# Performance work log

Hardware: AMD Instinct MI355X
Metric: run time of the kernel (lower is better)

## Reference

```python
import jax, jax.numpy as jnp
import numpy as np

N = 131072
IN_A = 256
IN_V = 512
IN_VF = 512
CH = 256
BN_EPS = 1e-5
COS_EPS = 1e-8


def setup_inputs() -> dict:
    key = jax.random.key(0)
    ks = jax.random.split(key, 12)
    s = 0.05
    return {
        "x": jax.random.normal(ks[0], (N, 4, 512), dtype=jnp.float32),
        "audio_node_mask": jax.random.bernoulli(ks[1], 0.5, (N,)),
        "W_a": jax.random.normal(ks[2], (IN_A, CH), dtype=jnp.float32) * s,
        "b_a": jnp.zeros((CH,), jnp.float32),
        "W_v": jax.random.normal(ks[3], (IN_V, CH), dtype=jnp.float32) * s,
        "b_v": jnp.zeros((CH,), jnp.float32),
        "W_f": jax.random.normal(ks[4], (2 * CH, CH), dtype=jnp.float32) * s,
        "b_f": jnp.zeros((CH,), jnp.float32),
        "gamma": jnp.ones((CH,), jnp.float32),
        "beta": jnp.zeros((CH,), jnp.float32),
        "W_fc": jax.random.normal(ks[5], (CH, 2), dtype=jnp.float32) * s,
        "b_fc": jnp.zeros((2,), jnp.float32),
    }


def reference(x, audio_node_mask, W_a, b_a, W_v, b_v, W_f, b_f, gamma, beta, W_fc, b_fc):
    # Slice per-type features (x: [N, 4, 512])
    a_in = x[:, 0, :IN_A]    # audio feats (also video->audio feats)
    v_in = x[:, 1, :IN_V]    # video feats
    a_vf = x[:, 2, :IN_VF]   # audio voice-face emb
    v_vf = x[:, 3, :IN_VF]   # video voice-face emb

    # cosine similarity along feature dim (torch.nn.functional.cosine_similarity semantics)
    dot = jnp.sum(a_vf * v_vf, axis=1)
    denom = jnp.maximum(jnp.linalg.norm(a_vf, axis=1) * jnp.linalg.norm(v_vf, axis=1), COS_EPS)
    sim = dot / denom  # [N]

    # per-type linears (compute densely, select by mask -> same math as masked scatter)
    a_out = a_in @ W_a + b_a                                   # [N, CH]
    v_out = v_in @ W_v + b_v                                   # [N, CH]
    va = a_in * sim[:, None]                                   # sim-weighted audio feats on video nodes
    fused = jnp.concatenate([va, v_out], axis=1) @ W_f + b_f   # [N, CH]

    graph_feats = jnp.where(audio_node_mask[:, None], a_out, fused)

    # BatchNorm1d (training: batch statistics, biased variance)
    mu = jnp.mean(graph_feats, axis=0)
    var = jnp.mean(jnp.square(graph_feats - mu), axis=0)
    graph_feats = (graph_feats - mu) * jax.lax.rsqrt(var + BN_EPS) * gamma + beta

    graph_feats = jax.nn.relu(graph_feats)
    return graph_feats @ W_fc + b_fc  # [N, 2]
```

## Files before the change

### kernel.cpp

```cpp
#include <hip/hip_runtime.h>
#include <hip/hip_bf16.h>
#include <stdint.h>

#define NN 131072

typedef unsigned int uint;
typedef unsigned short ushort;
typedef __attribute__((ext_vector_type(8))) __bf16 bf16x8;
typedef __attribute__((ext_vector_type(2))) __bf16 bf16x2;
typedef __attribute__((ext_vector_type(4))) float f32x4;


__device__ __forceinline__ ushort f2bf(float f) {
    uint u = __float_as_uint(f);
    u += 0x7FFF + ((u >> 16) & 1);
    return (ushort)(u >> 16);
}
__device__ __forceinline__ uint pk2(float a, float b) {
    bf16x2 t;
    t[0] = (__bf16)a;
    t[1] = (__bf16)b;
    return __builtin_bit_cast(uint, t);
}
__device__ __forceinline__ bool mask_val(const unsigned char* m8, int flag, int i) {
    return flag ? (m8[(size_t)i * 4] != 0) : (m8[i] != 0);
}
__device__ __forceinline__ size_t pack_off(int k, int c) {
    return (size_t)(((k >> 5) * 16 + (c >> 4)) * 512
                    + (((k >> 3) & 3) * 16 + (c & 15)) * 8 + (k & 7));
}

__global__ void k_detect(const uint* m32, int n, int* flag) {
    __shared__ int cnt;
    if (threadIdx.x == 0) cnt = 0;
    __syncthreads();
    int local = 0;
    int nw = n >> 2;
    for (int i = threadIdx.x; i < nw; i += 1024)
        if (m32[i] & 0x0000FF00u) local = 1;
    if (local) atomicAdd(&cnt, 1);
    __syncthreads();
    if (threadIdx.x == 0) *flag = (cnt == 0) ? 1 : 0;
}

__global__ void k_count(const unsigned char* m8, const int* flagp, int* cntM) {
    int flag = *flagp;
    int t = threadIdx.x;
    bool m = mask_val(m8, flag, blockIdx.x * 256 + t);
    unsigned long long bal = __ballot(m);
    __shared__ int wsum[4];
    if ((t & 63) == 0) wsum[t >> 6] = __popcll(bal);
    __syncthreads();
    if (t == 0) cntM[blockIdx.x] = wsum[0] + wsum[1] + wsum[2] + wsum[3];
}

__global__ void k_scan(const int* __restrict__ cntM, int* __restrict__ meta,
                       int* __restrict__ baseA, int* __restrict__ baseF) {
    __shared__ int sA[512], sF[512];
    int t = threadIdx.x;
    int a = cntM[t], f = 256 - a;
    sA[t] = a; sF[t] = f;
    __syncthreads();
    for (int off = 1; off < 512; off <<= 1) {
        int va = (t >= off) ? sA[t - off] : 0;
        int vf = (t >= off) ? sF[t - off] : 0;
        __syncthreads();
        sA[t] += va; sF[t] += vf;
        __syncthreads();
    }
    baseA[t] = sA[t] - a;
    baseF[t] = sF[t] - f;
    if (t == 511) { meta[2] = sA[511]; meta[1] = sF[511]; }
}

__global__ void k_fill(const unsigned char* m8, const int* flagp,
                       const int* __restrict__ baseA, const int* __restrict__ baseF,
                       int* __restrict__ audioIdx, int* __restrict__ fusedIdx) {
    int flag = *flagp;
    int blk = blockIdx.x, t = threadIdx.x;
    int row = blk * 256 + t;
    bool m = mask_val(m8, flag, row);
    unsigned long long bal = __ballot(m);
    int lane = t & 63, w = t >> 6;
    unsigned long long lt = (1ull << lane) - 1ull;
    int pA = __popcll(bal & lt);
    __shared__ int wA[4];
    if (lane == 0) wA[w] = __popcll(bal);
    __syncthreads();
    int offA = 0;
    for (int i = 0; i < w; ++i) offA += wA[i];
    int offF = w * 64 - offA;
    int pF = lane - pA;
    if (m) audioIdx[baseA[blk] + offA + pA] = row;
    else   fusedIdx[baseF[blk] + offF + pF] = row;
}

__global__ void k_prep(const float* __restrict__ Wa, const float* __restrict__ Wf,
                       const float* __restrict__ Wv, const float* __restrict__ bv,
                       const float* __restrict__ bf_, ushort* __restrict__ Bwa,
                       ushort* __restrict__ Bwf, float* __restrict__ cf) {
    int c = threadIdx.x;
    int b = blockIdx.x;
    if (b < 256) {
        Bwa[pack_off(b, c)] = f2bf(Wa[b * 256 + c]);
    } else if (b < 512) {
        Bwf[pack_off(512 + (b - 256), c)] = f2bf(Wf[(b - 256) * 256 + c]);
    } else if (b < 1024) {
        int k = b - 512;
        const float* wr = Wv + k * 256;
        float acc = 0.f;
        for (int j = 0; j < 256; ++j) acc += wr[j] * Wf[(256 + j) * 256 + c];
        Bwf[pack_off(k, c)] = f2bf(acc);
    } else {
        float acc = bf_[c];
        for (int j = 0; j < 256; ++j) acc += bv[j] * Wf[(256 + j) * 256 + c];
        cf[c] = acc;
    }
}

__global__ __launch_bounds__(512, 4) void k_main(
    const float* __restrict__ x, const int* __restrict__ meta,
    const int* __restrict__ fusedIdx, const int* __restrict__ audioIdx,
    const ushort* __restrict__ Bwa, const ushort* __restrict__ Bwf,
    const float* __restrict__ ba, const float* __restrict__ cf,
    ushort* __restrict__ gf, float* __restrict__ bn_s, float* __restrict__ bn_q)
{
    __shared__ bf16x8 As8[2][128 * 8];
    __shared__ int ridxS[128];
    __shared__ float simS[128];
    __shared__ unsigned char validS[128];
    __shared__ float redS[256], redQ[256];

    const int tid = threadIdx.x;
    const int cntF = meta[1], cntA = meta[2];
    const int nbF = (cntF + 127) >> 7;
    const int nbA = (cntA + 127) >> 7;
    const int b = blockIdx.x;
    const bool isF = b < nbF;
    const int bb = isF ? b : b - nbF;

    if (!isF && bb >= nbA) {
        if (tid < 256) {
            bn_s[(size_t)b * 256 + tid] = 0.f;
            bn_q[(size_t)b * 256 + tid] = 0.f;
        }
        return;
    }

    const int cnt = isF ? cntF : cntA;
    const int* idxArr = isF ? fusedIdx : audioIdx;
    const int lane = tid & 63;
    const int w = tid >> 6, wr = w >> 2, wc = w & 3;
    const int fr = lane & 15, fg = lane >> 4;

    if (tid < 128) {
        int gpos = bb * 128 + tid;
        int ok = gpos < cnt;
        ridxS[tid] = ok ? idxArr[gpos] : 0;
        validS[tid] = ok;
        simS[tid] = 1.f;
    }
    __syncthreads();

    const int NS = isF ? 12 : 4;
    const int sr = tid >> 2, sk = tid & 3;
    const float* xrow = x + (size_t)ridxS[sr] * 2048;
    const float sVf = validS[sr] ? 1.f : 0.f;
    float sAf = 0.f;

    int4 pA_A[2], pA_B[2];
    auto loadA = [&](int st, int4* p) {
        const float scl = (isF && st >= 8) ? sAf : sVf;
        const int off = isF ? ((st < 8) ? 512 + st * 64 : (st - 8) * 64) : st * 64;
        const float4* src = (const float4*)(xrow + off + sk * 16);
        #pragma unroll
        for (int s = 0; s < 2; ++s) {
            float4 u0 = src[2 * s], u1 = src[2 * s + 1];
            int4 q;
            q.x = pk2(u0.x * scl, u0.y * scl);
            q.y = pk2(u0.z * scl, u0.w * scl);
            q.z = pk2(u1.x * scl, u1.y * scl);
            q.w = pk2(u1.z * scl, u1.w * scl);
            p[s] = q;
        }
    };
    auto storeA = [&](int buf, const int4* p) {
        #pragma unroll
        for (int s = 0; s < 2; ++s)
            As8[buf][sr * 8 + ((sk * 2 + s) ^ (sr & 7))] = __builtin_bit_cast(bf16x8, p[s]);
    };

    const ushort* bBase = (isF ? Bwf : Bwa) + ((size_t)(wc * 4) << 9) + (lane << 3);

    f32x4 acc[4][4];
    #pragma unroll
    for (int m = 0; m < 4; ++m)
        #pragma unroll
        for (int n = 0; n < 4; ++n) acc[m][n] = (f32x4){0.f, 0.f, 0.f, 0.f};

    auto compute = [&](int buf, int st) {
        #pragma unroll
        for (int kk = 0; kk < 2; ++kk) {
            bf16x8 af[4];
            #pragma unroll
            for (int m = 0; m < 4; ++m) {
                int r = wr * 64 + m * 16 + fr;
                af[m] = As8[buf][r * 8 + ((kk * 4 + fg) ^ (r & 7))];
            }
            #pragma unroll
            for (int n = 0; n < 4; ++n) {
                bf16x8 bv = *(const bf16x8*)(bBase + ((size_t)((st * 2 + kk) * 16 + n) << 9));
                #pragma unroll
                for (int m = 0; m < 4; ++m)
                    acc[m][n] = __builtin_amdgcn_mfma_f32_16x16x32_bf16(
                        af[m], bv, acc[m][n], 0, 0, 0);
            }
        }
    };

    loadA(0, pA_A);

    if (isF) {
        #pragma unroll 2
        for (int rr = 0; rr < 16; ++rr) {
            int r = w * 16 + rr;
            const float4* p = (const float4*)(x + (size_t)ridxS[r] * 2048 + 1024);
            float4 a0 = p[lane], a1 = p[lane + 64];
            float4 v0 = p[lane + 128], v1 = p[lane + 192];
            float dot = a0.x * v0.x + a0.y * v0.y + a0.z * v0.z + a0.w * v0.w
                      + a1.x * v1.x + a1.y * v1.y + a1.z * v1.z + a1.w * v1.w;
            float na = a0.x * a0.x + a0.y * a0.y + a0.z * a0.z + a0.w * a0.w
                     + a1.x * a1.x + a1.y * a1.y + a1.z * a1.z + a1.w * a1.w;
            float nv = v0.x * v0.x + v0.y * v0.y + v0.z * v0.z + v0.w * v0.w
                     + v1.x * v1.x + v1.y * v1.y + v1.z * v1.z + v1.w * v1.w;
            #pragma unroll
            for (int off = 32; off; off >>= 1) {
                dot += __shfl_xor(dot, off);
                na  += __shfl_xor(na,  off);
                nv  += __shfl_xor(nv,  off);
            }
            if (lane == 0)
                simS[r] = dot / fmaxf(sqrtf(na) * sqrtf(nv), 1e-8f);
        }
    }
    __syncthreads();
    sAf = validS[sr] ? simS[sr] : 0.f;

    storeA(0, pA_A);
    loadA(1, pA_B);
    __syncthreads();

    for (int st = 0; st < NS; st += 2) {
        if (st + 2 < NS) loadA(st + 2, pA_A);
        compute(0, st);
        storeA(1, pA_B);
        __syncthreads();
        if (st + 3 < NS) loadA(st + 3, pA_B);
        compute(1, st + 1);
        if (st + 2 < NS) storeA(0, pA_A);
        __syncthreads();
    }

    if (tid < 256) { redS[tid] = 0.f; redQ[tid] = 0.f; }
    __syncthreads();

    const int colLo = wc * 64 + fr;
    const float* biasp = isF ? cf : ba;
    float bN[4];
    #pragma unroll
    for (int n = 0; n < 4; ++n) bN[n] = biasp[colLo + n * 16];

    float cs[4] = {0.f, 0.f, 0.f, 0.f}, cq[4] = {0.f, 0.f, 0.f, 0.f};
    #pragma unroll
    for (int m = 0; m < 4; ++m) {
        #pragma unroll
        for (int j = 0; j < 4; ++j) {
            int rloc = wr * 64 + m * 16 + fg * 4 + j;
            if (!validS[rloc]) continue;
            ushort* grow = gf + (size_t)ridxS[rloc] * 256;
            #pragma unroll
            for (int n = 0; n < 4; ++n) {
                float g = acc[m][n][j] + bN[n];
                grow[colLo + n * 16] = f2bf(g);
                cs[n] += g;
                cq[n] += g * g;
            }
        }
    }
    #pragma unroll
    for (int n = 0; n < 4; ++n) {
        atomicAdd(&redS[colLo + n * 16], cs[n]);
        atomicAdd(&redQ[colLo + n * 16], cq[n]);
    }
    __syncthreads();
    if (tid < 256) {
        bn_s[(size_t)b * 256 + tid] = redS[tid];
        bn_q[(size_t)b * 256 + tid] = redQ[tid];
    }
}

__global__ void k_stats(const float* __restrict__ bn_s, const float* __restrict__ bn_q,
                        const float* __restrict__ gamma, const float* __restrict__ beta,
                        float* __restrict__ scale, float* __restrict__ shift) {
    int c = blockIdx.x;
    int t = threadIdx.x;
    float s = 0.f, q = 0.f;
    for (int r = t; r < 1025; r += 256) {
        s += bn_s[(size_t)r * 256 + c];
        q += bn_q[(size_t)r * 256 + c];
    }
    __shared__ float ss[256], qq[256];
    ss[t] = s; qq[t] = q;
    __syncthreads();
    for (int off = 128; off; off >>= 1) {
        if (t < off) { ss[t] += ss[t + off]; qq[t] += qq[t + off]; }
        __syncthreads();
    }
    if (t == 0) {
        float mu  = ss[0] / 131072.f;
        float var = qq[0] / 131072.f - mu * mu;
        float sc = gamma[c] * rsqrtf(var + 1e-5f);
        scale[c] = sc;
        shift[c] = beta[c] - mu * sc;
    }
}

__global__ void k_out(const ushort* __restrict__ gf, const float* __restrict__ scale,
                      const float* __restrict__ shift, const float* __restrict__ Wfc,
                      const float* __restrict__ bfc, float* __restrict__ out) {
    int wid = threadIdx.x >> 6;
    int lane = threadIdx.x & 63;
    int i = blockIdx.x * 4 + wid;
    uint2 gv = ((const uint2*)(gf + (size_t)i * 256))[lane];
    float g0 = __uint_as_float(gv.x << 16);
    float g1 = __uint_as_float(gv.x & 0xFFFF0000u);
    float g2 = __uint_as_float(gv.y << 16);
    float g3 = __uint_as_float(gv.y & 0xFFFF0000u);
    int c0 = lane * 4;
    float4 sc = *(const float4*)(scale + c0);
    float4 sh = *(const float4*)(shift + c0);
    float y0 = fmaxf(g0 * sc.x + sh.x, 0.f);
    float y1 = fmaxf(g1 * sc.y + sh.y, 0.f);
    float y2 = fmaxf(g2 * sc.z + sh.z, 0.f);
    float y3 = fmaxf(g3 * sc.w + sh.w, 0.f);
    const float4* w = (const float4*)(Wfc + c0 * 2);
    float4 w0 = w[0], w1 = w[1];
    float p0 = y0 * w0.x + y1 * w0.z + y2 * w1.x + y3 * w1.z;
    float p1 = y0 * w0.y + y1 * w0.w + y2 * w1.y + y3 * w1.w;
    #pragma unroll
    for (int off = 32; off; off >>= 1) {
        p0 += __shfl_xor(p0, off);
        p1 += __shfl_xor(p1, off);
    }
    if (lane == 0) {
        out[(size_t)i * 2]     = p0 + bfc[0];
        out[(size_t)i * 2 + 1] = p1 + bfc[1];
    }
}

extern "C" void kernel_launch(void* const* d_in, const int* in_sizes, int n_in,
                              void* d_out, int out_size, void* d_ws, size_t ws_size,
                              hipStream_t stream) {
    const float* x          = (const float*)d_in[0];
    const unsigned char* mk = (const unsigned char*)d_in[1];
    const float* Wa  = (const float*)d_in[2];
    const float* ba  = (const float*)d_in[3];
    const float* Wv  = (const float*)d_in[4];
    const float* bv  = (const float*)d_in[5];
    const float* Wf  = (const float*)d_in[6];
    const float* bf  = (const float*)d_in[7];
    const float* gamma = (const float*)d_in[8];
    const float* beta  = (const float*)d_in[9];
    const float* Wfc = (const float*)d_in[10];
    const float* bfc = (const float*)d_in[11];
    float* out = (float*)d_out;

    char* ws = (char*)d_ws;
    int*    meta   = (int*)ws;
    float*  scale  = (float*)(ws + 1024);
    float*  shift  = (float*)(ws + 2048);
    float*  cf     = (float*)(ws + 3072);
    int*    cntM   = (int*)(ws + 8192);
    int*    baseA  = (int*)(ws + 12288);
    int*    baseF  = (int*)(ws + 16384);
    ushort* Bwa    = (ushort*)(ws + 32768);
    ushort* Bwf    = (ushort*)(ws + 262144);
    int*    fusedIdx = (int*)(ws + (1u << 20));
    int*    audioIdx = (int*)(ws + (1u << 20) + (512u << 10));
    float*  bn_s   = (float*)(ws + (2u << 20));
    float*  bn_q   = (float*)(ws + (4u << 20));
    ushort* gf     = (ushort*)(ws + (8u << 20));

    int n = in_sizes[1];

    k_detect<<<1, 1024, 0, stream>>>((const uint*)mk, n, meta);
    k_count<<<512, 256, 0, stream>>>(mk, meta, cntM);
    k_scan<<<1, 512, 0, stream>>>(cntM, meta, baseA, baseF);
    k_fill<<<512, 256, 0, stream>>>(mk, meta, baseA, baseF, audioIdx, fusedIdx);
    k_prep<<<1025, 256, 0, stream>>>(Wa, Wf, Wv, bv, bf, Bwa, Bwf, cf);
    k_main<<<1025, 512, 0, stream>>>(x, meta, fusedIdx, audioIdx, Bwa, Bwf, ba, cf,
                                     gf, bn_s, bn_q);
    k_stats<<<256, 256, 0, stream>>>(bn_s, bn_q, gamma, beta, scale, shift);
    k_out<<<NN / 4, 256, 0, stream>>>(gf, scale, shift, Wfc, bfc, out);
}
```

Measured before the change: 245.1 us.

## Interleave cosine-sim with GEMM pipeline, stage output via LDS, vectorize mask detect

The cosine-similarity computation for fused rows is split into chunks and interleaved with the first seven K-steps of the bf16 MFMA main loop, so the similarity loads overlap with the matrix work instead of running before it. The double-buffer loop is rewritten with one register staging set and a single barrier per step. Output rows are staged through LDS and written to the gf buffer as 32-byte contiguous stores per row, replacing scattered 2-byte stores. The mask-detect kernel reads 16 bytes per thread instead of 4. The LDS staging adds extra barriers in the epilogue.

```diff
diff --git a/kernel.cpp b/kernel.cpp
--- a/kernel.cpp
+++ b/kernel.cpp
@@ -30,14 +30,16 @@
                     + (((k >> 3) & 3) * 16 + (c & 15)) * 8 + (k & 7));
 }
 
-__global__ void k_detect(const uint* m32, int n, int* flag) {
+__global__ void k_detect(const uint4* m128, int n, int* flag) {
     __shared__ int cnt;
     if (threadIdx.x == 0) cnt = 0;
     __syncthreads();
     int local = 0;
-    int nw = n >> 2;
-    for (int i = threadIdx.x; i < nw; i += 1024)
-        if (m32[i] & 0x0000FF00u) local = 1;
+    int nv = n >> 4;
+    for (int i = threadIdx.x; i < nv; i += 1024) {
+        uint4 v = m128[i];
+        if ((v.x | v.y | v.z | v.w) & 0x0000FF00u) local = 1;
+    }
     if (local) atomicAdd(&cnt, 1);
     __syncthreads();
     if (threadIdx.x == 0) *flag = (cnt == 0) ? 1 : 0;
@@ -168,8 +170,8 @@
     const float sVf = validS[sr] ? 1.f : 0.f;
     float sAf = 0.f;
 
-    int4 pA_A[2], pA_B[2];
-    auto loadA = [&](int st, int4* p) {
+    int4 pA[2];
+    auto loadA = [&](int st) {
         const float scl = (isF && st >= 8) ? sAf : sVf;
         const int off = isF ? ((st < 8) ? 512 + st * 64 : (st - 8) * 64) : st * 64;
         const float4* src = (const float4*)(xrow + off + sk * 16);
@@ -181,49 +183,19 @@
             q.y = pk2(u0.z * scl, u0.w * scl);
             q.z = pk2(u1.x * scl, u1.y * scl);
             q.w = pk2(u1.z * scl, u1.w * scl);
-            p[s] = q;
+            pA[s] = q;
         }
     };
-    auto storeA = [&](int buf, const int4* p) {
+    auto storeA = [&](int buf) {
         #pragma unroll
         for (int s = 0; s < 2; ++s)
-            As8[buf][sr * 8 + ((sk * 2 + s) ^ (sr & 7))] = __builtin_bit_cast(bf16x8, p[s]);
+            As8[buf][sr * 8 + ((sk * 2 + s) ^ (sr & 7))] = __builtin_bit_cast(bf16x8, pA[s]);
     };
 
-    const ushort* bBase = (isF ? Bwf : Bwa) + ((size_t)(wc * 4) << 9) + (lane << 3);
-
-    f32x4 acc[4][4];
-    #pragma unroll
-    for (int m = 0; m < 4; ++m)
-        #pragma unroll
-        for (int n = 0; n < 4; ++n) acc[m][n] = (f32x4){0.f, 0.f, 0.f, 0.f};
-
-    auto compute = [&](int buf, int st) {
-        #pragma unroll
-        for (int kk = 0; kk < 2; ++kk) {
-            bf16x8 af[4];
-            #pragma unroll
-            for (int m = 0; m < 4; ++m) {
-                int r = wr * 64 + m * 16 + fr;
-                af[m] = As8[buf][r * 8 + ((kk * 4 + fg) ^ (r & 7))];
-            }
-            #pragma unroll
-            for (int n = 0; n < 4; ++n) {
-                bf16x8 bv = *(const bf16x8*)(bBase + ((size_t)((st * 2 + kk) * 16 + n) << 9));
-                #pragma unroll
-                for (int m = 0; m < 4; ++m)
-                    acc[m][n] = __builtin_amdgcn_mfma_f32_16x16x32_bf16(
-                        af[m], bv, acc[m][n], 0, 0, 0);
-            }
-        }
-    };
-
-    loadA(0, pA_A);
-
-    if (isF) {
-        #pragma unroll 2
-        for (int rr = 0; rr < 16; ++rr) {
-            int r = w * 16 + rr;
+    auto simChunk = [&](int q) {
+        #pragma unroll
+        for (int rr = 0; rr < 2; ++rr) {
+            int r = w * 16 + q * 2 + rr;
             const float4* p = (const float4*)(x + (size_t)ridxS[r] * 2048 + 1024);
             float4 a0 = p[lane], a1 = p[lane + 64];
             float4 v0 = p[lane + 128], v1 = p[lane + 192];
@@ -242,51 +214,92 @@
             if (lane == 0)
                 simS[r] = dot / fmaxf(sqrtf(na) * sqrtf(nv), 1e-8f);
         }
-    }
-    __syncthreads();
-    sAf = validS[sr] ? simS[sr] : 0.f;
-
-    storeA(0, pA_A);
-    loadA(1, pA_B);
-    __syncthreads();
-
-    for (int st = 0; st < NS; st += 2) {
-        if (st + 2 < NS) loadA(st + 2, pA_A);
-        compute(0, st);
-        storeA(1, pA_B);
-        __syncthreads();
-        if (st + 3 < NS) loadA(st + 3, pA_B);
-        compute(1, st + 1);
-        if (st + 2 < NS) storeA(0, pA_A);
-        __syncthreads();
+    };
+
+    const ushort* bBase = (isF ? Bwf : Bwa) + ((size_t)(wc * 4) << 9) + (lane << 3);
+
+    f32x4 acc[4][4];
+    #pragma unroll
+    for (int m = 0; m < 4; ++m)
+        #pragma unroll
+        for (int n = 0; n < 4; ++n) acc[m][n] = (f32x4){0.f, 0.f, 0.f, 0.f};
+
+    auto compute = [&](int buf, int st) {
+        #pragma unroll
+        for (int kk = 0; kk < 2; ++kk) {
+            bf16x8 af[4];
+            #pragma unroll
+            for (int m = 0; m < 4; ++m) {
+                int r = wr * 64 + m * 16 + fr;
+                af[m] = As8[buf][r * 8 + ((kk * 4 + fg) ^ (r & 7))];
+            }
+            #pragma unroll
+            for (int n = 0; n < 4; ++n) {
+                bf16x8 bv = *(const bf16x8*)(bBase + ((size_t)((st * 2 + kk) * 16 + n) << 9));
+                #pragma unroll
+                for (int m = 0; m < 4; ++m)
+                    acc[m][n] = __builtin_amdgcn_mfma_f32_16x16x32_bf16(
+                        af[m], bv, acc[m][n], 0, 0, 0);
+            }
+        }
+    };
+
+    loadA(0);
+    if (isF) simChunk(0);
+    storeA(0);
+    __syncthreads();
+
+    for (int st = 0; st < NS; ++st) {
+        if (st + 1 < NS) loadA(st + 1);
+        if (isF && st < 7) simChunk(st + 1);
+        compute(st & 1, st);
+        if (st + 1 < NS) storeA((st + 1) & 1);
+        __syncthreads();
+        if (st == 6) sAf = validS[sr] ? simS[sr] : 0.f;
     }
 
     if (tid < 256) { redS[tid] = 0.f; redQ[tid] = 0.f; }
-    __syncthreads();
-
     const int colLo = wc * 64 + fr;
     const float* biasp = isF ? cf : ba;
     float bN[4];
     #pragma unroll
     for (int n = 0; n < 4; ++n) bN[n] = biasp[colLo + n * 16];
-
     float cs[4] = {0.f, 0.f, 0.f, 0.f}, cq[4] = {0.f, 0.f, 0.f, 0.f};
+
+    ushort* tile = (ushort*)As8;
+    const int rslot = tid >> 4;
+    const int cb = (tid & 15) * 16;
+    const int rloc2 = (rslot >> 4) * 64 + (rslot & 15);
+    __syncthreads();
+
     #pragma unroll
     for (int m = 0; m < 4; ++m) {
         #pragma unroll
         for (int j = 0; j < 4; ++j) {
+            int slot = wr * 16 + fg * 4 + j;
             int rloc = wr * 64 + m * 16 + fg * 4 + j;
-            if (!validS[rloc]) continue;
-            ushort* grow = gf + (size_t)ridxS[rloc] * 256;
-            #pragma unroll
-            for (int n = 0; n < 4; ++n) {
-                float g = acc[m][n][j] + bN[n];
-                grow[colLo + n * 16] = f2bf(g);
-                cs[n] += g;
-                cq[n] += g * g;
+            if (validS[rloc]) {
+                #pragma unroll
+                for (int n = 0; n < 4; ++n) {
+                    float g = acc[m][n][j] + bN[n];
+                    tile[slot * 264 + colLo + n * 16] = f2bf(g);
+                    cs[n] += g;
+                    cq[n] += g * g;
+                }
             }
         }
-    }
+        __syncthreads();
+        int rg = rloc2 + m * 16;
+        if (validS[rg]) {
+            const uint4* tp = (const uint4*)(tile + rslot * 264 + cb);
+            uint4 v0 = tp[0], v1 = tp[1];
+            ushort* grow = gf + (size_t)ridxS[rg] * 256 + cb;
+            *(uint4*)grow = v0;
+            *(uint4*)(grow + 8) = v1;
+        }
+        __syncthreads();
+    }
+
     #pragma unroll
     for (int n = 0; n < 4; ++n) {
         atomicAdd(&redS[colLo + n * 16], cs[n]);
@@ -393,7 +406,7 @@
 
     int n = in_sizes[1];
 
-    k_detect<<<1, 1024, 0, stream>>>((const uint*)mk, n, meta);
+    k_detect<<<1, 1024, 0, stream>>>((const uint4*)mk, n, meta);
     k_count<<<512, 256, 0, stream>>>(mk, meta, cntM);
     k_scan<<<1, 512, 0, stream>>>(cntM, meta, baseA, baseF);
     k_fill<<<512, 256, 0, stream>>>(mk, meta, baseA, baseF, audioIdx, fusedIdx);
```

New measurement: 264.5 us. 1.08x slower.
